# Kernel tuning notes

Measured on AMD Instinct MI355X. Metric: run time of the kernel, lower is better.

## Reference

```python
import jax, jax.numpy as jnp
import numpy as np

B, NT, NW, D, H = 32768, 10, 3, 64, 4
EPS = 1e-5

def _ln(x, g, b):
    mu = jnp.mean(x, axis=-1, keepdims=True)
    var = jnp.mean((x - mu) ** 2, axis=-1, keepdims=True)
    return (x - mu) * jax.lax.rsqrt(var + EPS) * g + b

def _mha(q_in, kv, wq, bq, wk, bk, wv, bv, wo, bo):
    Bb, Lq, Dm = q_in.shape
    Lk = kv.shape[1]
    dh = Dm // H
    q = (q_in @ wq + bq).reshape(Bb, Lq, H, dh)
    k = (kv @ wk + bk).reshape(Bb, Lk, H, dh)
    v = (kv @ wv + bv).reshape(Bb, Lk, H, dh)
    s = jnp.einsum('bqhd,bkhd->bhqk', q, k) / np.float32(np.sqrt(dh))
    a = jax.nn.softmax(s, axis=-1)
    o = jnp.einsum('bhqk,bkhd->bqhd', a, v).reshape(Bb, Lq, Dm)
    return o @ wo + bo

def setup_inputs() -> dict:
    key = jax.random.key(0)
    ks = iter(jax.random.split(key, 40))
    def rn(shape, scale=0.05):
        return jax.random.normal(next(ks), shape, dtype=jnp.float32) * scale
    inp = {
        'track_left': jax.random.normal(next(ks), (B, NT, 2), dtype=jnp.float32),
        'track_right': jax.random.normal(next(ks), (B, NT, 2), dtype=jnp.float32),
        'qemb': rn((NW, D), 1.0),
        'ip_w1': rn((2, D // 2)), 'ip_b1': jnp.zeros((D // 2,), jnp.float32),
        'ip_w2': rn((D // 2, D)), 'ip_b2': jnp.zeros((D,), jnp.float32),
    }
    for p in ('a1', 'a2'):
        for nm in ('wq', 'wk', 'wv', 'wo'):
            inp[p + '_' + nm] = rn((D, D))
        for nm in ('bq', 'bk', 'bv', 'bo'):
            inp[p + '_' + nm] = jnp.zeros((D,), jnp.float32)
    inp['ffn_w1'] = rn((D, 2 * D)); inp['ffn_b1'] = jnp.zeros((2 * D,), jnp.float32)
    inp['ffn_w2'] = rn((2 * D, D)); inp['ffn_b2'] = jnp.zeros((D,), jnp.float32)
    for n in ('n1', 'n2', 'n3'):
        inp[n + '_g'] = jnp.ones((D,), jnp.float32)
        inp[n + '_b'] = jnp.zeros((D,), jnp.float32)
    inp['op_w1'] = rn((D, D // 2)); inp['op_b1'] = jnp.zeros((D // 2,), jnp.float32)
    inp['op_w2'] = rn((D // 2, 2)); inp['op_b2'] = jnp.zeros((2,), jnp.float32)
    return inp

def reference(track_left, track_right, qemb, ip_w1, ip_b1, ip_w2, ip_b2,
              a1_wq, a1_bq, a1_wk, a1_bk, a1_wv, a1_bv, a1_wo, a1_bo,
              a2_wq, a2_bq, a2_wk, a2_bk, a2_wv, a2_bv, a2_wo, a2_bo,
              ffn_w1, ffn_b1, ffn_w2, ffn_b2,
              n1_g, n1_b, n2_g, n2_b, n3_g, n3_b,
              op_w1, op_b1, op_w2, op_b2):
    # concat left/right boundaries -> [B, 2*NT, 2]
    pts = jnp.concatenate([track_left, track_right], axis=1)
    # input projection MLP -> [B, 2*NT, D]
    feats = jax.nn.relu(pts @ ip_w1 + ip_b1) @ ip_w2 + ip_b2
    # learned waypoint queries broadcast over batch -> [B, NW, D]
    q0 = jnp.broadcast_to(qemb[None], (pts.shape[0], NW, D))
    x1 = _ln(q0 + _mha(q0, feats, a1_wq, a1_bq, a1_wk, a1_bk, a1_wv, a1_bv, a1_wo, a1_bo), n1_g, n1_b)
    x2 = _ln(x1 + _mha(x1, feats, a2_wq, a2_bq, a2_wk, a2_bk, a2_wv, a2_bv, a2_wo, a2_bo), n2_g, n2_b)
    f = jax.nn.relu(x2 @ ffn_w1 + ffn_b1) @ ffn_w2 + ffn_b2
    x3 = _ln(x2 + f, n3_g, n3_b)
    # output projection -> [B, NW, 2]
    return jax.nn.relu(x3 @ op_w1 + op_b1) @ op_w2 + op_b2
```

## Files before the change

### kernel.cpp

```cpp
#include <hip/hip_runtime.h>
#include <math.h>

#define SCALE 0.36067376022224085f

#define WVF1F 0
#define WVF2F 2048
#define WKT2F 4096
#define G1F   6144
#define BVF1F 6528
#define BVF2F 6592
#define PQ2   6656
#define PO1   10752
#define PO2   14848
#define PV1   18944
#define PV2   20992
#define PF1   23040
#define PF2   31232
#define POP1  39424

#define WSYNC() do { asm volatile("s_waitcnt lgkmcnt(0)" ::: "memory"); __builtin_amdgcn_wave_barrier(); } while (0)

struct Params {
  const float* tl; const float* tr; const float* qemb;
  const float* ip_w1; const float* ip_b1;
  const float* bq2;
  const float* bo1; const float* bo2;
  const float* ffn_b1; const float* ffn_b2;
  const float* n1_g; const float* n1_b;
  const float* n2_g; const float* n2_b;
  const float* n3_g; const float* n3_b;
  const float* op_b1;
  const float* op_w2; const float* op_b2;
  const float* ws;
  float* out;
};

__global__ void prep1_kernel(const float* ip_w2, const float* ip_b2,
                             const float* wk2, const float* wv1, const float* wv2,
                             const float* bv1, const float* bv2, float* ws) {
  const int bid = blockIdx.x, tid = threadIdx.x;
  if (bid < 24) {
    const int idx = bid * 256 + tid;
    const int mat = idx >> 11;
    const int rem = idx & 2047;
    const int j = rem >> 6, c = rem & 63;
    const float* W = (mat == 0) ? wv1 : (mat == 1) ? wv2 : wk2;
    float acc = 0.f;
    for (int m = 0; m < 64; ++m) acc = fmaf(ip_w2[j * 64 + m], W[m * 64 + c], acc);
    if (mat == 0)      ws[WVF1F + j * 64 + c] = acc;
    else if (mat == 1) ws[WVF2F + j * 64 + c] = acc;
    else               ws[WKT2F + c * 32 + j] = acc * SCALE;
  } else if (tid < 128) {
    const int l = tid >> 6, d = tid & 63;
    const float* bv = l ? bv2 : bv1;
    const float* wv = l ? wv2 : wv1;
    float acc = bv[d];
    for (int m = 0; m < 64; ++m) acc = fmaf(ip_b2[m], wv[m * 64 + d], acc);
    ws[(l ? BVF2F : BVF1F) + d] = acc;
  }
}

__global__ void prep2_kernel(const float* ip_w2, const float* wk1,
                             const float* qemb, const float* wq1, const float* bq1,
                             float* ws) {
  __shared__ float wkf[32][64];
  __shared__ float q1[3][64];
  const int tid = threadIdx.x;
  for (int e = tid; e < 2048; e += 384) {
    const int j = e >> 6, c = e & 63;
    float acc = 0.f;
    for (int m = 0; m < 64; ++m) acc = fmaf(ip_w2[j * 64 + m], wk1[m * 64 + c], acc);
    wkf[j][c] = acc;
  }
  if (tid < 192) {
    const int q = tid >> 6, d = tid & 63;
    float acc = bq1[d];
    for (int e = 0; e < 64; ++e) acc = fmaf(qemb[q * 64 + e], wq1[e * 64 + d], acc);
    q1[q][d] = acc;
  }
  __syncthreads();
  {
    const int r = tid >> 5, j = tid & 31;
    const int h = r / 3, q = r - h * 3;
    float acc = 0.f;
    for (int d = 0; d < 16; ++d) acc = fmaf(wkf[j][h * 16 + d], q1[q][h * 16 + d], acc);
    ws[G1F + r * 32 + j] = acc * SCALE;
  }
}

__global__ void prepC_kernel(float* ws,
                             const float* wq2, const float* wo1, const float* wo2,
                             const float* fw1, const float* fw2, const float* opw1) {
  const int e = blockIdx.x * 256 + threadIdx.x;
  if (e >= 34816) return;
  float v; int dst;
  if (e < 4096) {
    const int i = e, jc = i >> 8, rem = i & 255, d = rem >> 2, r = rem & 3;
    v = wq2[(jc * 4 + r) * 64 + d]; dst = PQ2 + i;
  } else if (e < 8192) {
    const int i = e - 4096, jc = i >> 8, rem = i & 255, d = rem >> 2, r = rem & 3;
    v = wo1[(jc * 4 + r) * 64 + d]; dst = PO1 + i;
  } else if (e < 12288) {
    const int i = e - 8192, jc = i >> 8, rem = i & 255, d = rem >> 2, r = rem & 3;
    v = wo2[(jc * 4 + r) * 64 + d]; dst = PO2 + i;
  } else if (e < 14336) {
    const int i = e - 12288, jc = i >> 8, rem = i & 255, d = rem >> 2, r = rem & 3;
    v = ws[WVF1F + (jc * 4 + r) * 64 + d]; dst = PV1 + i;
  } else if (e < 16384) {
    const int i = e - 14336, jc = i >> 8, rem = i & 255, d = rem >> 2, r = rem & 3;
    v = ws[WVF2F + (jc * 4 + r) * 64 + d]; dst = PV2 + i;
  } else if (e < 24576) {
    const int i = e - 16384, jc = i >> 9, rem = i & 511, d = rem >> 2, r = rem & 3;
    v = fw1[(jc * 4 + r) * 128 + d]; dst = PF1 + i;
  } else if (e < 32768) {
    const int i = e - 24576, mc = i >> 8, rem = i & 255, d = rem >> 2, r = rem & 3;
    v = fw2[(mc * 4 + r) * 64 + d]; dst = PF2 + i;
  } else {
    const int i = e - 32768, jc = i >> 7, rem = i & 127, d = rem >> 2, r = rem & 3;
    v = opw1[(jc * 4 + r) * 32 + d]; dst = POP1 + i;
  }
  ws[dst] = v;
}

__global__ __launch_bounds__(256) void planner_kernel(Params p) {
  const int w = threadIdx.x >> 6;
  const int lane = threadIdx.x & 63;
  const int item = blockIdx.x * 4 + w;

  __shared__ __align__(16) float g1_s[12][36];
  __shared__ __align__(16) float a_s[4][20][36];
  __shared__ __align__(16) float att_s[4][12][24];
  __shared__ __align__(16) float ch_s[4][12][36];
  __shared__ __align__(16) float qx_s[4][3][68];
  __shared__ __align__(16) float x_s[4][3][68];
  __shared__ float pts_s[4][40];

  const float* ws = p.ws;

  for (int e = threadIdx.x; e < 384; e += 256)
    g1_s[e >> 5][e & 31] = ws[G1F + e];

  if (lane < 40)
    pts_s[w][lane] = (lane < 20) ? p.tl[item * 20 + lane] : p.tr[item * 20 + lane - 20];
  WSYNC();

  {
    const int j = lane & 31, th = lane >> 5;
    const float w0 = p.ip_w1[j], w1 = p.ip_w1[32 + j], b = p.ip_b1[j];
#pragma unroll
    for (int i = 0; i < 10; ++i) {
      const int t = th * 10 + i;
      a_s[w][t][j] = fmaxf(fmaf(pts_s[w][2 * t], w0, fmaf(pts_s[w][2 * t + 1], w1, b)), 0.f);
    }
  }
  __syncthreads();

  const int t3 = lane / 3;
  const int q3 = lane - t3 * 3;
  const int j32 = lane & 31, half = lane >> 5, hq0 = half * 6;
  const int h16 = lane >> 4;

  float xq[3];

#pragma unroll
  for (int l = 0; l < 2; ++l) {
    if (l == 1) {
      float acc[3];
#pragma unroll
      for (int q = 0; q < 3; ++q) acc[q] = p.bq2[lane];
#pragma unroll
      for (int jc = 0; jc < 16; ++jc) {
        const float4 w4 = *(const float4*)&ws[PQ2 + jc * 256 + lane * 4];
#pragma unroll
        for (int q = 0; q < 3; ++q) {
          const float4 xv = *(const float4*)&x_s[w][q][jc * 4];
          acc[q] = fmaf(xv.x, w4.x, fmaf(xv.y, w4.y, fmaf(xv.z, w4.z, fmaf(xv.w, w4.w, acc[q]))));
        }
      }
#pragma unroll
      for (int q = 0; q < 3; ++q) qx_s[w][q][lane] = acc[q];
      WSYNC();
      {
        float g2[6] = {0, 0, 0, 0, 0, 0};
        const int D0 = half * 32;
#pragma unroll
        for (int dd = 0; dd < 32; ++dd) {
          const int D = D0 + dd;
          const float wk = ws[WKT2F + D * 32 + j32];
          const int hl = dd >> 4;
#pragma unroll
          for (int q = 0; q < 3; ++q)
            g2[hl * 3 + q] = fmaf(wk, qx_s[w][q][D], g2[hl * 3 + q]);
        }
#pragma unroll
        for (int k = 0; k < 6; ++k) ch_s[w][hq0 + k][j32] = g2[k];
      }
      WSYNC();
    }

    const float (*g)[36] = (l == 0) ? (const float (*)[36])g1_s : (const float (*)[36])ch_s[w];
    if (lane < 60) {
      float acc[4] = {0, 0, 0, 0};
#pragma unroll
      for (int jc = 0; jc < 8; ++jc) {
        const float4 av = *(const float4*)&a_s[w][t3][jc * 4];
#pragma unroll
        for (int h = 0; h < 4; ++h) {
          const float4 gv = *(const float4*)&g[h * 3 + q3][jc * 4];
          acc[h] = fmaf(av.x, gv.x, fmaf(av.y, gv.y, fmaf(av.z, gv.z, fmaf(av.w, gv.w, acc[h]))));
        }
      }
#pragma unroll
      for (int h = 0; h < 4; ++h) att_s[w][h * 3 + q3][t3] = acc[h];
    }
    WSYNC();

    if (lane < 12) {
      float m = -1e30f;
#pragma unroll
      for (int t = 0; t < 20; ++t) m = fmaxf(m, att_s[w][lane][t]);
      float s = 0.f;
#pragma unroll
      for (int t = 0; t < 20; ++t) {
        const float e = exp2f(att_s[w][lane][t] - m);
        att_s[w][lane][t] = e;
        s += e;
      }
      att_s[w][lane][20] = 1.f / s;
    }
    WSYNC();

    {
      float c[6] = {0, 0, 0, 0, 0, 0};
#pragma unroll
      for (int tc = 0; tc < 5; ++tc) {
        float av[4];
#pragma unroll
        for (int r = 0; r < 4; ++r) av[r] = a_s[w][tc * 4 + r][j32];
#pragma unroll
        for (int k = 0; k < 6; ++k) {
          const float4 at = *(const float4*)&att_s[w][hq0 + k][tc * 4];
          c[k] = fmaf(at.x, av[0], fmaf(at.y, av[1], fmaf(at.z, av[2], fmaf(at.w, av[3], c[k]))));
        }
      }
#pragma unroll
      for (int k = 0; k < 6; ++k)
        ch_s[w][hq0 + k][j32] = c[k] * att_s[w][hq0 + k][20];
    }
    WSYNC();

    {
      const int pv = l ? PV2 : PV1;
      const float bv = ws[(l ? BVF2F : BVF1F) + lane];
      float o[3] = {bv, bv, bv};
#pragma unroll
      for (int jc = 0; jc < 8; ++jc) {
        const float4 w4 = *(const float4*)&ws[pv + jc * 256 + lane * 4];
#pragma unroll
        for (int q = 0; q < 3; ++q) {
          const float4 cv = *(const float4*)&ch_s[w][h16 * 3 + q][jc * 4];
          o[q] = fmaf(cv.x, w4.x, fmaf(cv.y, w4.y, fmaf(cv.z, w4.z, fmaf(cv.w, w4.w, o[q]))));
        }
      }
#pragma unroll
      for (int q = 0; q < 3; ++q) qx_s[w][q][lane] = o[q];
    }
    WSYNC();

    {
      const int po = l ? PO2 : PO1;
      const float* bo = l ? p.bo2 : p.bo1;
      const float* gg = l ? p.n2_g : p.n1_g;
      const float* gb = l ? p.n2_b : p.n1_b;
      float acc[3];
#pragma unroll
      for (int q = 0; q < 3; ++q)
        acc[q] = bo[lane] + (l ? x_s[w][q][lane] : p.qemb[q * 64 + lane]);
#pragma unroll
      for (int jc = 0; jc < 16; ++jc) {
        const float4 w4 = *(const float4*)&ws[po + jc * 256 + lane * 4];
#pragma unroll
        for (int q = 0; q < 3; ++q) {
          const float4 ov = *(const float4*)&qx_s[w][q][jc * 4];
          acc[q] = fmaf(ov.x, w4.x, fmaf(ov.y, w4.y, fmaf(ov.z, w4.z, fmaf(ov.w, w4.w, acc[q]))));
        }
      }
      const float gv = gg[lane], bv = gb[lane];
#pragma unroll
      for (int q = 0; q < 3; ++q) {
        const float v = acc[q];
        float s = v;
#pragma unroll
        for (int m = 32; m >= 1; m >>= 1) s += __shfl_xor(s, m);
        const float mu = s * (1.f / 64.f);
        const float d = v - mu;
        float s2 = d * d;
#pragma unroll
        for (int m = 32; m >= 1; m >>= 1) s2 += __shfl_xor(s2, m);
        const float inv = rsqrtf(s2 * (1.f / 64.f) + 1e-5f);
        const float xn = fmaf(d * inv, gv, bv);
        xq[q] = xn;
        x_s[w][q][lane] = xn;
      }
    }
    WSYNC();
  }

  float* f1p = (float*)a_s[w];
  {
    float a0[3], a1[3];
    const float b0 = p.ffn_b1[lane], b1 = p.ffn_b1[64 + lane];
#pragma unroll
    for (int q = 0; q < 3; ++q) { a0[q] = b0; a1[q] = b1; }
#pragma unroll
    for (int jc = 0; jc < 16; ++jc) {
      const float4 w04 = *(const float4*)&ws[PF1 + jc * 512 + lane * 4];
      const float4 w14 = *(const float4*)&ws[PF1 + jc * 512 + 256 + lane * 4];
#pragma unroll
      for (int q = 0; q < 3; ++q) {
        const float4 xv = *(const float4*)&x_s[w][q][jc * 4];
        a0[q] = fmaf(xv.x, w04.x, fmaf(xv.y, w04.y, fmaf(xv.z, w04.z, fmaf(xv.w, w04.w, a0[q]))));
        a1[q] = fmaf(xv.x, w14.x, fmaf(xv.y, w14.y, fmaf(xv.z, w14.z, fmaf(xv.w, w14.w, a1[q]))));
      }
    }
#pragma unroll
    for (int q = 0; q < 3; ++q) {
      f1p[q * 136 + lane] = fmaxf(a0[q], 0.f);
      f1p[q * 136 + 64 + lane] = fmaxf(a1[q], 0.f);
    }
  }
  WSYNC();

  {
    float acc[3];
#pragma unroll
    for (int q = 0; q < 3; ++q) acc[q] = p.ffn_b2[lane] + xq[q];
#pragma unroll
    for (int mc = 0; mc < 32; ++mc) {
      const float4 w4 = *(const float4*)&ws[PF2 + mc * 256 + lane * 4];
#pragma unroll
      for (int q = 0; q < 3; ++q) {
        const float4 fv = *(const float4*)&f1p[q * 136 + mc * 4];
        acc[q] = fmaf(fv.x, w4.x, fmaf(fv.y, w4.y, fmaf(fv.z, w4.z, fmaf(fv.w, w4.w, acc[q]))));
      }
    }
    const float gv = p.n3_g[lane], bv = p.n3_b[lane];
#pragma unroll
    for (int q = 0; q < 3; ++q) {
      const float v = acc[q];
      float s = v;
#pragma unroll
      for (int m = 32; m >= 1; m >>= 1) s += __shfl_xor(s, m);
      const float mu = s * (1.f / 64.f);
      const float d = v - mu;
      float s2 = d * d;
#pragma unroll
      for (int m = 32; m >= 1; m >>= 1) s2 += __shfl_xor(s2, m);
      const float inv = rsqrtf(s2 * (1.f / 64.f) + 1e-5f);
      x_s[w][q][lane] = fmaf(d * inv, gv, bv);
    }
  }
  WSYNC();

  if (lane < 32) {
    float acc[3];
#pragma unroll
    for (int q = 0; q < 3; ++q) acc[q] = p.op_b1[lane];
#pragma unroll
    for (int jc = 0; jc < 16; ++jc) {
      const float4 w4 = *(const float4*)&ws[POP1 + jc * 128 + lane * 4];
#pragma unroll
      for (int q = 0; q < 3; ++q) {
        const float4 xv = *(const float4*)&x_s[w][q][jc * 4];
        acc[q] = fmaf(xv.x, w4.x, fmaf(xv.y, w4.y, fmaf(xv.z, w4.z, fmaf(xv.w, w4.w, acc[q]))));
      }
    }
#pragma unroll
    for (int q = 0; q < 3; ++q) qx_s[w][q][lane] = fmaxf(acc[q], 0.f);
  }
  WSYNC();

  if (lane < 6) {
    const int q = lane >> 1, e = lane & 1;
    float acc = p.op_b2[e];
#pragma unroll
    for (int m = 0; m < 32; ++m) acc = fmaf(qx_s[w][q][m], p.op_w2[m * 2 + e], acc);
    p.out[item * 6 + q * 2 + e] = acc;
  }
}

extern "C" void kernel_launch(void* const* d_in, const int* in_sizes, int n_in,
                              void* d_out, int out_size, void* d_ws, size_t ws_size,
                              hipStream_t stream) {
  const float* in[40];
  for (int i = 0; i < n_in && i < 40; ++i) in[i] = (const float*)d_in[i];

  const float *a1_wq, *a1_wk, *a1_wv, *a1_wo, *a1_bq, *a1_bk, *a1_bv, *a1_bo;
  const float *a2_wq, *a2_wk, *a2_wv, *a2_wo, *a2_bq, *a2_bk, *a2_bv, *a2_bo;
  if (in_sizes[8] == 4096) {
    a1_wq = in[7];  a1_wk = in[8];  a1_wv = in[9];  a1_wo = in[10];
    a1_bq = in[11]; a1_bk = in[12]; a1_bv = in[13]; a1_bo = in[14];
    a2_wq = in[15]; a2_wk = in[16]; a2_wv = in[17]; a2_wo = in[18];
    a2_bq = in[19]; a2_bk = in[20]; a2_bv = in[21]; a2_bo = in[22];
  } else {
    a1_wq = in[7];  a1_bq = in[8];  a1_wk = in[9];  a1_bk = in[10];
    a1_wv = in[11]; a1_bv = in[12]; a1_wo = in[13]; a1_bo = in[14];
    a2_wq = in[15]; a2_bq = in[16]; a2_wk = in[17]; a2_bk = in[18];
    a2_wv = in[19]; a2_bv = in[20]; a2_wo = in[21]; a2_bo = in[22];
  }
  (void)a1_bk; (void)a2_bk;

  float* ws = (float*)d_ws;
  prep1_kernel<<<25, 256, 0, stream>>>(in[5], in[6], a2_wk, a1_wv, a2_wv, a1_bv, a2_bv, ws);
  prep2_kernel<<<1, 384, 0, stream>>>(in[5], a1_wk, in[2], a1_wq, a1_bq, ws);
  prepC_kernel<<<136, 256, 0, stream>>>(ws, a2_wq, a1_wo, a2_wo, in[23], in[25], in[33]);

  Params p;
  p.tl = in[0]; p.tr = in[1]; p.qemb = in[2];
  p.ip_w1 = in[3]; p.ip_b1 = in[4];
  p.bq2 = a2_bq;
  p.bo1 = a1_bo; p.bo2 = a2_bo;
  p.ffn_b1 = in[24]; p.ffn_b2 = in[26];
  p.n1_g = in[27]; p.n1_b = in[28]; p.n2_g = in[29]; p.n2_b = in[30];
  p.n3_g = in[31]; p.n3_b = in[32];
  p.op_b1 = in[34]; p.op_w2 = in[35]; p.op_b2 = in[36];
  p.ws = ws; p.out = (float*)d_out;

  planner_kernel<<<8192, 256, 0, stream>>>(p);
}
```

Measured before the change: 238.4 us.

## Prefetch next-stage weights before barriers and parallelize softmax and output reductions

Issues global loads for the first two float4 weight chunks of each upcoming matmul stage before the preceding wave sync, so their latency overlaps the current stage. Adds a row-major copy of the scaled K-fold matrix so the score-projection loop can use float4 loads. Spreads the softmax over 4 lanes per row with shuffle reductions, and normalizes in place instead of storing a reciprocal. Also splits the final output dot product across 4 lanes. In exchange it uses more registers, which may lower occupancy, and adds extra workspace.

```diff
diff --git a/kernel.cpp b/kernel.cpp
--- a/kernel.cpp
+++ b/kernel.cpp
@@ -17,6 +17,7 @@
 #define PF1   23040
 #define PF2   31232
 #define POP1  39424
+#define PKT2F 41472
 
 #define WSYNC() do { asm volatile("s_waitcnt lgkmcnt(0)" ::: "memory"); __builtin_amdgcn_wave_barrier(); } while (0)
 
@@ -49,7 +50,10 @@
     for (int m = 0; m < 64; ++m) acc = fmaf(ip_w2[j * 64 + m], W[m * 64 + c], acc);
     if (mat == 0)      ws[WVF1F + j * 64 + c] = acc;
     else if (mat == 1) ws[WVF2F + j * 64 + c] = acc;
-    else               ws[WKT2F + c * 32 + j] = acc * SCALE;
+    else {
+      ws[WKT2F + c * 32 + j] = acc * SCALE;
+      ws[PKT2F + j * 64 + c] = acc * SCALE;
+    }
   } else if (tid < 128) {
     const int l = tid >> 6, d = tid & 63;
     const float* bv = l ? bv2 : bv1;
@@ -159,8 +163,10 @@
   const int q3 = lane - t3 * 3;
   const int j32 = lane & 31, half = lane >> 5, hq0 = half * 6;
   const int h16 = lane >> 4;
+  const int r12 = lane >> 2, sub = lane & 3;
 
   float xq[3];
+  float4 pv0, pv1, po0, po1, pn0, pn1, pk0, pk1, pf20, pf21, ph0;
 
 #pragma unroll
   for (int l = 0; l < 2; ++l) {
@@ -170,7 +176,8 @@
       for (int q = 0; q < 3; ++q) acc[q] = p.bq2[lane];
 #pragma unroll
       for (int jc = 0; jc < 16; ++jc) {
-        const float4 w4 = *(const float4*)&ws[PQ2 + jc * 256 + lane * 4];
+        const float4 w4 = (jc == 0) ? pn0 : (jc == 1) ? pn1
+                        : *(const float4*)&ws[PQ2 + jc * 256 + lane * 4];
 #pragma unroll
         for (int q = 0; q < 3; ++q) {
           const float4 xv = *(const float4*)&x_s[w][q][jc * 4];
@@ -179,18 +186,24 @@
       }
 #pragma unroll
       for (int q = 0; q < 3; ++q) qx_s[w][q][lane] = acc[q];
+      pk0 = *(const float4*)&ws[PKT2F + j32 * 64 + half * 32 + 0];
+      pk1 = *(const float4*)&ws[PKT2F + j32 * 64 + half * 32 + 4];
       WSYNC();
       {
         float g2[6] = {0, 0, 0, 0, 0, 0};
         const int D0 = half * 32;
-#pragma unroll
-        for (int dd = 0; dd < 32; ++dd) {
-          const int D = D0 + dd;
-          const float wk = ws[WKT2F + D * 32 + j32];
-          const int hl = dd >> 4;
-#pragma unroll
-          for (int q = 0; q < 3; ++q)
-            g2[hl * 3 + q] = fmaf(wk, qx_s[w][q][D], g2[hl * 3 + q]);
+        const float* pkt = &ws[PKT2F + j32 * 64 + D0];
+#pragma unroll
+        for (int dd = 0; dd < 8; ++dd) {
+          const float4 wk4 = (dd == 0) ? pk0 : (dd == 1) ? pk1
+                           : *(const float4*)&pkt[dd * 4];
+          const int hl = dd >> 2;
+#pragma unroll
+          for (int q = 0; q < 3; ++q) {
+            const float4 q4 = *(const float4*)&qx_s[w][q][D0 + dd * 4];
+            g2[hl * 3 + q] = fmaf(q4.x, wk4.x, fmaf(q4.y, wk4.y,
+                              fmaf(q4.z, wk4.z, fmaf(q4.w, wk4.w, g2[hl * 3 + q]))));
+          }
         }
 #pragma unroll
         for (int k = 0; k < 6; ++k) ch_s[w][hq0 + k][j32] = g2[k];
@@ -215,18 +228,30 @@
     }
     WSYNC();
 
-    if (lane < 12) {
-      float m = -1e30f;
-#pragma unroll
-      for (int t = 0; t < 20; ++t) m = fmaxf(m, att_s[w][lane][t]);
-      float s = 0.f;
-#pragma unroll
-      for (int t = 0; t < 20; ++t) {
-        const float e = exp2f(att_s[w][lane][t] - m);
-        att_s[w][lane][t] = e;
-        s += e;
-      }
-      att_s[w][lane][20] = 1.f / s;
+    if (r12 < 12) {
+      const int tb = sub * 5;
+      float v0 = att_s[w][r12][tb],     v1 = att_s[w][r12][tb + 1];
+      float v2 = att_s[w][r12][tb + 2], v3 = att_s[w][r12][tb + 3];
+      float v4 = att_s[w][r12][tb + 4];
+      float m = fmaxf(fmaxf(fmaxf(v0, v1), fmaxf(v2, v3)), v4);
+      m = fmaxf(m, __shfl_xor(m, 1));
+      m = fmaxf(m, __shfl_xor(m, 2));
+      v0 = exp2f(v0 - m); v1 = exp2f(v1 - m); v2 = exp2f(v2 - m);
+      v3 = exp2f(v3 - m); v4 = exp2f(v4 - m);
+      float s = v0 + v1 + v2 + v3 + v4;
+      s += __shfl_xor(s, 1);
+      s += __shfl_xor(s, 2);
+      const float inv = 1.f / s;
+      att_s[w][r12][tb]     = v0 * inv;
+      att_s[w][r12][tb + 1] = v1 * inv;
+      att_s[w][r12][tb + 2] = v2 * inv;
+      att_s[w][r12][tb + 3] = v3 * inv;
+      att_s[w][r12][tb + 4] = v4 * inv;
+    }
+    {
+      const int pvo = l ? PV2 : PV1;
+      pv0 = *(const float4*)&ws[pvo + lane * 4];
+      pv1 = *(const float4*)&ws[pvo + 256 + lane * 4];
     }
     WSYNC();
 
@@ -244,18 +269,23 @@
         }
       }
 #pragma unroll
-      for (int k = 0; k < 6; ++k)
-        ch_s[w][hq0 + k][j32] = c[k] * att_s[w][hq0 + k][20];
+      for (int k = 0; k < 6; ++k) ch_s[w][hq0 + k][j32] = c[k];
+    }
+    {
+      const int poo = l ? PO2 : PO1;
+      po0 = *(const float4*)&ws[poo + lane * 4];
+      po1 = *(const float4*)&ws[poo + 256 + lane * 4];
     }
     WSYNC();
 
     {
-      const int pv = l ? PV2 : PV1;
+      const int pvo = l ? PV2 : PV1;
       const float bv = ws[(l ? BVF2F : BVF1F) + lane];
       float o[3] = {bv, bv, bv};
 #pragma unroll
       for (int jc = 0; jc < 8; ++jc) {
-        const float4 w4 = *(const float4*)&ws[pv + jc * 256 + lane * 4];
+        const float4 w4 = (jc == 0) ? pv0 : (jc == 1) ? pv1
+                        : *(const float4*)&ws[pvo + jc * 256 + lane * 4];
 #pragma unroll
         for (int q = 0; q < 3; ++q) {
           const float4 cv = *(const float4*)&ch_s[w][h16 * 3 + q][jc * 4];
@@ -265,10 +295,17 @@
 #pragma unroll
       for (int q = 0; q < 3; ++q) qx_s[w][q][lane] = o[q];
     }
+    if (l == 0) {
+      pn0 = *(const float4*)&ws[PQ2 + lane * 4];
+      pn1 = *(const float4*)&ws[PQ2 + 256 + lane * 4];
+    } else {
+      pn0 = *(const float4*)&ws[PF1 + lane * 4];
+      pn1 = *(const float4*)&ws[PF1 + 256 + lane * 4];
+    }
     WSYNC();
 
     {
-      const int po = l ? PO2 : PO1;
+      const int poo = l ? PO2 : PO1;
       const float* bo = l ? p.bo2 : p.bo1;
       const float* gg = l ? p.n2_g : p.n1_g;
       const float* gb = l ? p.n2_b : p.n1_b;
@@ -278,7 +315,8 @@
         acc[q] = bo[lane] + (l ? x_s[w][q][lane] : p.qemb[q * 64 + lane]);
 #pragma unroll
       for (int jc = 0; jc < 16; ++jc) {
-        const float4 w4 = *(const float4*)&ws[po + jc * 256 + lane * 4];
+        const float4 w4 = (jc == 0) ? po0 : (jc == 1) ? po1
+                        : *(const float4*)&ws[poo + jc * 256 + lane * 4];
 #pragma unroll
         for (int q = 0; q < 3; ++q) {
           const float4 ov = *(const float4*)&qx_s[w][q][jc * 4];
@@ -314,8 +352,8 @@
     for (int q = 0; q < 3; ++q) { a0[q] = b0; a1[q] = b1; }
 #pragma unroll
     for (int jc = 0; jc < 16; ++jc) {
-      const float4 w04 = *(const float4*)&ws[PF1 + jc * 512 + lane * 4];
-      const float4 w14 = *(const float4*)&ws[PF1 + jc * 512 + 256 + lane * 4];
+      const float4 w04 = (jc == 0) ? pn0 : *(const float4*)&ws[PF1 + jc * 512 + lane * 4];
+      const float4 w14 = (jc == 0) ? pn1 : *(const float4*)&ws[PF1 + jc * 512 + 256 + lane * 4];
 #pragma unroll
       for (int q = 0; q < 3; ++q) {
         const float4 xv = *(const float4*)&x_s[w][q][jc * 4];
@@ -329,6 +367,8 @@
       f1p[q * 136 + 64 + lane] = fmaxf(a1[q], 0.f);
     }
   }
+  pf20 = *(const float4*)&ws[PF2 + lane * 4];
+  pf21 = *(const float4*)&ws[PF2 + 256 + lane * 4];
   WSYNC();
 
   {
@@ -337,7 +377,8 @@
     for (int q = 0; q < 3; ++q) acc[q] = p.ffn_b2[lane] + xq[q];
 #pragma unroll
     for (int mc = 0; mc < 32; ++mc) {
-      const float4 w4 = *(const float4*)&ws[PF2 + mc * 256 + lane * 4];
+      const float4 w4 = (mc == 0) ? pf20 : (mc == 1) ? pf21
+                      : *(const float4*)&ws[PF2 + mc * 256 + lane * 4];
 #pragma unroll
       for (int q = 0; q < 3; ++q) {
         const float4 fv = *(const float4*)&f1p[q * 136 + mc * 4];
@@ -360,6 +401,7 @@
       x_s[w][q][lane] = fmaf(d * inv, gv, bv);
     }
   }
+  ph0 = *(const float4*)&ws[POP1 + lane * 4];
   WSYNC();
 
   if (lane < 32) {
@@ -368,7 +410,7 @@
     for (int q = 0; q < 3; ++q) acc[q] = p.op_b1[lane];
 #pragma unroll
     for (int jc = 0; jc < 16; ++jc) {
-      const float4 w4 = *(const float4*)&ws[POP1 + jc * 128 + lane * 4];
+      const float4 w4 = (jc == 0) ? ph0 : *(const float4*)&ws[POP1 + jc * 128 + lane * 4];
 #pragma unroll
       for (int q = 0; q < 3; ++q) {
         const float4 xv = *(const float4*)&x_s[w][q][jc * 4];
@@ -380,12 +422,18 @@
   }
   WSYNC();
 
-  if (lane < 6) {
-    const int q = lane >> 1, e = lane & 1;
-    float acc = p.op_b2[e];
-#pragma unroll
-    for (int m = 0; m < 32; ++m) acc = fmaf(qx_s[w][q][m], p.op_w2[m * 2 + e], acc);
-    p.out[item * 6 + q * 2 + e] = acc;
+  if (lane < 24) {
+    const int q = lane >> 3, e = (lane >> 2) & 1, mg = lane & 3;
+    float acc = 0.f;
+#pragma unroll
+    for (int k = 0; k < 8; ++k) {
+      const int m = mg * 8 + k;
+      acc = fmaf(qx_s[w][q][m], p.op_w2[m * 2 + e], acc);
+    }
+    acc += __shfl_xor(acc, 1);
+    acc += __shfl_xor(acc, 2);
+    if (mg == 0)
+      p.out[item * 6 + q * 2 + e] = acc + p.op_b2[e];
   }
 }
 
```

Measured after the change: 239.1 us. About the same (+0.3%).
